# Performance work log

Hardware: AMD Instinct MI355X
Metric: run time of the kernel (lower is better)

The kernel has to match this reference:

```python
import jax, jax.numpy as jnp
import numpy as np

EPS = 1e-8
TAU = 10.0
SCALE = 1.0
PH, PW = 5, 5  # patch_size; stride == patch_size (module default)
CX, CY = PH // 2, PW // 2


def _split_into_patches(x):
    """[B, C, H, W] -> [B, C, L, ph, pw] with non-overlapping ph x pw patches
    (stride == patch size, matching the module's default patch_stride)."""
    B, C, H, W = x.shape
    Hp, Wp = H // PH, W // PW
    x = x[:, :, : Hp * PH, : Wp * PW].reshape(B, C, Hp, PH, Wp, PW)
    x = x.transpose(0, 1, 2, 4, 3, 5)  # [B, C, Hp, Wp, ph, pw]
    return x.reshape(B, C, Hp * Wp, PH, PW)


def setup_inputs() -> dict:
    key = jax.random.key(0)
    k1, k2 = jax.random.split(key)
    seg_feat = jax.random.normal(k1, (4, 64, 512, 512), dtype=jnp.float32)
    dep_true = jax.random.uniform(k2, (4, 1, 512, 512), dtype=jnp.float32) * 80.0
    return {"seg_feat": seg_feat, "dep_true": dep_true}


def reference(seg_feat, dep_true):
    seg_feat = seg_feat.astype(jnp.float32)
    dep_true = dep_true.astype(jnp.float32)

    # --- depth branch (no_grad in the original) ---
    dep_patch = _split_into_patches(dep_true)[:, 0]          # [B, L, ph, pw]
    dep_valid = dep_patch > EPS
    dep_center = dep_patch[:, :, CX, CY][:, :, None, None]   # [B, L, 1, 1]
    dep_diff = jnp.abs(dep_center - dep_patch)               # [B, L, ph, pw]

    # --- segmentation branch ---
    seg_patch = _split_into_patches(seg_feat)                # [B, C, L, ph, pw]
    seg_center = seg_patch[:, :, :, CX, CY][:, :, :, None, None]
    seg_sq = jnp.sum((seg_center - seg_patch) ** 2, axis=1)  # [B, L, ph, pw] = seg_diff**2

    # exp(-seg_diff**2) == exp(-seg_sq); avoids sqrt in the differentiable path
    loss = jnp.exp(-dep_diff / TAU) * jnp.exp(-seg_sq)

    # --- mask (no_grad in the original) ---
    seg_diff = jnp.sqrt(seg_sq)
    mask = (dep_diff > EPS) & (seg_diff > EPS) & dep_valid
    mask = mask.at[:, :, CX, CY].set(False)

    # masked_select(...).mean()
    n = jnp.maximum(jnp.sum(mask), 1)
    mean = jnp.sum(jnp.where(mask, loss, 0.0)) / n.astype(loss.dtype)
    return mean * SCALE
```

## Files before the change

kernel.cpp:

```cpp
#include <hip/hip_runtime.h>
#include <math.h>


#define EPSF 1e-8f
#define PH 5
#define HPATCH 102
#define HH 512
#define WW 512
#define CC 64
#define HW (HH * WW)

__global__ __launch_bounds__(320) void dgp_main(const float* __restrict__ seg,
                                                const float* __restrict__ dep,
                                                float* __restrict__ ws) {
  const int bid = blockIdx.x;
  const int q   = bid & 3;
  const int hp  = (bid >> 2) % HPATCH;
  const int b   = (bid >> 2) / HPATCH;
  const int h0  = hp * PH;
  const int hc  = h0 + 2;
  const int qbase = q * 128;

  const int wp0   = qbase / PH;
  const int wpend = min((qbase + 127) / PH, HPATCH - 1);
  const int nwp   = wpend - wp0 + 1;

  __shared__ float s_cent[27 * 65];
  __shared__ float s_depc[27];
  __shared__ float s_red[10];

  const int tid = threadIdx.x;
  const long seg_b = (long)b * CC * HW;

  {
    const int grp = tid >> 5;
    const int wpl = tid & 31;
    if (wpl < nwp) {
      const long base = seg_b + (long)hc * WW + (wp0 + wpl) * PH + 2;
      for (int c = grp; c < CC; c += 10) {
        s_cent[wpl * 65 + c] = seg[base + (long)c * HW];
      }
    }
    if (tid < nwp) {
      s_depc[tid] = dep[((long)b * HH + hc) * WW + (wp0 + tid) * PH + 2];
    }
  }
  __syncthreads();

  const int row  = tid >> 6;
  const int lane = tid & 63;
  const int col0 = qbase + lane * 2;

  int w0 = min(col0 / PH - wp0, nwp - 1);
  int w1 = min((col0 + 1) / PH - wp0, nwp - 1);

  const float* cb0 = s_cent + w0 * 65;
  const float* cb1 = s_cent + w1 * 65;

  float acc0 = 0.f, acc1 = 0.f;
  const float* p = seg + seg_b + (long)(h0 + row) * WW + col0;

#pragma unroll 8
  for (int c = 0; c < CC; ++c) {
    float2 v = *(const float2*)(p + (long)c * HW);
    float d0 = cb0[c] - v.x;
    float d1 = cb1[c] - v.y;
    acc0 = fmaf(d0, d0, acc0);
    acc1 = fmaf(d1, d1, acc1);
  }

  float2 dv = *(const float2*)(dep + ((long)b * HH + h0 + row) * WW + col0);
  float dvals[2] = {dv.x, dv.y};
  float accs[2]  = {acc0, acc1};
  int wls[2]     = {w0, w1};

  float lsum = 0.f, lcnt = 0.f;
#pragma unroll
  for (int j = 0; j < 2; ++j) {
    int col = col0 + j;
    if (col < 510) {
      float dval = dvals[j];
      float dd   = fabsf(s_depc[wls[j]] - dval);
      float ssq  = accs[j];
      bool is_center = (row == 2) && (col % PH == 2);
      bool m = (dd > EPSF) && (ssq > EPSF * EPSF) && (dval > EPSF) && !is_center;
      if (m) {
        lsum += __expf(-(dd * 0.1f + ssq));
        lcnt += 1.f;
      }
    }
  }

#pragma unroll
  for (int off = 32; off > 0; off >>= 1) {
    lsum += __shfl_down(lsum, off, 64);
    lcnt += __shfl_down(lcnt, off, 64);
  }
  if (lane == 0) {
    s_red[row]     = lsum;
    s_red[5 + row] = lcnt;
  }
  __syncthreads();
  if (tid == 0) {
    float a = 0.f, n = 0.f;
#pragma unroll
    for (int w = 0; w < 5; ++w) {
      a += s_red[w];
      n += s_red[5 + w];
    }
    atomicAdd(&ws[0], a);
    atomicAdd(&ws[1], n);
  }
}

__global__ void dgp_final(const float* __restrict__ ws, float* __restrict__ out) {
  out[0] = ws[0] / fmaxf(ws[1], 1.0f);
}

extern "C" void kernel_launch(void* const* d_in, const int* in_sizes, int n_in,
                              void* d_out, int out_size, void* d_ws, size_t ws_size,
                              hipStream_t stream) {
  const float* seg = (const float*)d_in[0];
  const float* dep = (const float*)d_in[1];
  float* out = (float*)d_out;
  float* ws  = (float*)d_ws;

  hipMemsetAsync(d_ws, 0, 2 * sizeof(float), stream);

  const int nblocks = 4 * HPATCH * 4;
  dgp_main<<<dim3(nblocks), dim3(320), 0, stream>>>(seg, dep, ws);
  dgp_final<<<1, 1, 0, stream>>>(ws, out);
}
```

Before: 365.5 us.

## Process full patch-row per block with 8 columns per thread and float4 loads

Each block now covers a whole 512-wide patch row instead of a quarter, so the grid shrinks to 408 blocks and the per-patch center features are loaded into shared memory once per row. Each thread handles 8 contiguous columns with two float4 loads per channel instead of one float2. This is meant to cut redundant center-feature staging and raise memory-level parallelism per thread. In exchange, fewer blocks (408 on a 256-CU part) may leave CUs unevenly loaded, register pressure rises, and the staging loop has strided gathers.

```diff
diff --git a/kernel.cpp b/kernel.cpp
--- a/kernel.cpp
+++ b/kernel.cpp
@@ -14,75 +14,66 @@
                                                 const float* __restrict__ dep,
                                                 float* __restrict__ ws) {
   const int bid = blockIdx.x;
-  const int q   = bid & 3;
-  const int hp  = (bid >> 2) % HPATCH;
-  const int b   = (bid >> 2) / HPATCH;
+  const int hp  = bid % HPATCH;
+  const int b   = bid / HPATCH;
   const int h0  = hp * PH;
   const int hc  = h0 + 2;
-  const int qbase = q * 128;
-
-  const int wp0   = qbase / PH;
-  const int wpend = min((qbase + 127) / PH, HPATCH - 1);
-  const int nwp   = wpend - wp0 + 1;
-
-  __shared__ float s_cent[27 * 65];
-  __shared__ float s_depc[27];
-  __shared__ float s_red[10];
-
   const int tid = threadIdx.x;
   const long seg_b = (long)b * CC * HW;
 
-  {
-    const int grp = tid >> 5;
-    const int wpl = tid & 31;
-    if (wpl < nwp) {
-      const long base = seg_b + (long)hc * WW + (wp0 + wpl) * PH + 2;
-      for (int c = grp; c < CC; c += 10) {
-        s_cent[wpl * 65 + c] = seg[base + (long)c * HW];
-      }
-    }
-    if (tid < nwp) {
-      s_depc[tid] = dep[((long)b * HH + hc) * WW + (wp0 + tid) * PH + 2];
-    }
+  __shared__ float s_cent[CC * 103];
+  __shared__ float s_depc[HPATCH];
+  __shared__ float s_red[10];
+
+  for (int idx = tid; idx < CC * HPATCH; idx += 320) {
+    int c  = idx / HPATCH;
+    int wp = idx - c * HPATCH;
+    s_cent[c * 103 + wp] = seg[seg_b + (long)c * HW + (long)hc * WW + wp * PH + 2];
+  }
+  if (tid < HPATCH) {
+    s_depc[tid] = dep[((long)b * HH + hc) * WW + tid * PH + 2];
   }
   __syncthreads();
 
   const int row  = tid >> 6;
   const int lane = tid & 63;
-  const int col0 = qbase + lane * 2;
+  const int col0 = lane * 8;
+  const int h    = h0 + row;
 
-  int w0 = min(col0 / PH - wp0, nwp - 1);
-  int w1 = min((col0 + 1) / PH - wp0, nwp - 1);
+  int wp[8];
+#pragma unroll
+  for (int j = 0; j < 8; ++j) wp[j] = (col0 + j) / PH;
 
-  const float* cb0 = s_cent + w0 * 65;
-  const float* cb1 = s_cent + w1 * 65;
+  float acc[8] = {0.f, 0.f, 0.f, 0.f, 0.f, 0.f, 0.f, 0.f};
+  const float* p = seg + seg_b + (long)h * WW + col0;
 
-  float acc0 = 0.f, acc1 = 0.f;
-  const float* p = seg + seg_b + (long)(h0 + row) * WW + col0;
-
-#pragma unroll 8
+#pragma unroll 4
   for (int c = 0; c < CC; ++c) {
-    float2 v = *(const float2*)(p + (long)c * HW);
-    float d0 = cb0[c] - v.x;
-    float d1 = cb1[c] - v.y;
-    acc0 = fmaf(d0, d0, acc0);
-    acc1 = fmaf(d1, d1, acc1);
+    float4 v0 = *(const float4*)(p + (long)c * HW);
+    float4 v1 = *(const float4*)(p + (long)c * HW + 4);
+    const float* cb = s_cent + c * 103;
+    float vv[8] = {v0.x, v0.y, v0.z, v0.w, v1.x, v1.y, v1.z, v1.w};
+#pragma unroll
+    for (int j = 0; j < 8; ++j) {
+      float d = cb[wp[j]] - vv[j];
+      acc[j] = fmaf(d, d, acc[j]);
+    }
   }
 
-  float2 dv = *(const float2*)(dep + ((long)b * HH + h0 + row) * WW + col0);
-  float dvals[2] = {dv.x, dv.y};
-  float accs[2]  = {acc0, acc1};
-  int wls[2]     = {w0, w1};
+  const float* dp = dep + ((long)b * HH + h) * WW + col0;
+  float4 d0 = *(const float4*)dp;
+  float4 d1 = *(const float4*)(dp + 4);
+  float dv[8] = {d0.x, d0.y, d0.z, d0.w, d1.x, d1.y, d1.z, d1.w};
 
   float lsum = 0.f, lcnt = 0.f;
 #pragma unroll
-  for (int j = 0; j < 2; ++j) {
+  for (int j = 0; j < 8; ++j) {
     int col = col0 + j;
     if (col < 510) {
-      float dval = dvals[j];
-      float dd   = fabsf(s_depc[wls[j]] - dval);
-      float ssq  = accs[j];
-      bool is_center = (row == 2) && (col % PH == 2);
+      float dval = dv[j];
+      float dd   = fabsf(s_depc[wp[j]] - dval);
+      float ssq  = acc[j];
+      bool is_center = (row == 2) && (col - wp[j] * PH == 2);
       bool m = (dd > EPSF) && (ssq > EPSF * EPSF) && (dval > EPSF) && !is_center;
       if (m) {
         lsum += __expf(-(dd * 0.1f + ssq));
@@ -127,7 +118,7 @@
 
   hipMemsetAsync(d_ws, 0, 2 * sizeof(float), stream);
 
-  const int nblocks = 4 * HPATCH * 4;
+  const int nblocks = 4 * HPATCH;
   dgp_main<<<dim3(nblocks), dim3(320), 0, stream>>>(seg, dep, ws);
   dgp_final<<<1, 1, 0, stream>>>(ws, out);
 }
```

Measured after the change: 366.9 us. No clear change (+0.4%).
